# Optimization experiments

Measured on AMD Instinct MI355X. Metric: run time of the kernel, lower is better.

The kernel has to match this reference:

```python
import jax, jax.numpy as jnp
import numpy as np

S1, S2 = 1024, 1024
DA, DV, DOUT = 2, 64, 1
K1, K2 = 32, 32


def _gelu(x):
    # torch nn.GELU() default is the exact erf-based gelu
    return jax.nn.gelu(x, approximate=False)


def _flayer(Rr, Ri, w, x):
    f = jnp.fft.rfftn(x, axes=(0, 1))[:K1, :K2]            # [K1,K2,DV] complex
    Rf = jnp.einsum('abc,abcd->abd', f, Rr + 1j * Ri)       # [K1,K2,DV] complex
    kernelpart = jnp.fft.irfftn(Rf, s=(S1, S2), axes=(0, 1))  # [S1,S2,DV] real
    return _gelu(kernelpart + x @ w)


def setup_inputs() -> dict:
    key = jax.random.key(0)
    ks = jax.random.split(key, 20)
    d = {}
    d['input'] = jax.random.normal(ks[0], (S1, S2, DA), dtype=jnp.float32)
    d['Wsh'] = jax.random.normal(ks[1], (DA, DV), dtype=jnp.float32) * (1.0 / np.sqrt(DA))
    d['bsh'] = jax.random.normal(ks[2], (DV,), dtype=jnp.float32) * 0.02
    for i, base in zip(range(1, 5), range(3, 15, 3)):
        d[f'Rr{i}'] = jax.random.normal(ks[base], (K1, K2, DV, DV), dtype=jnp.float32) * (1.0 / DV)
        d[f'Ri{i}'] = jax.random.normal(ks[base + 1], (K1, K2, DV, DV), dtype=jnp.float32) * (1.0 / DV)
        d[f'w{i}'] = jax.random.normal(ks[base + 2], (DV, DV), dtype=jnp.float32) * (1.0 / np.sqrt(DV))
    d['Wp'] = jax.random.normal(ks[15], (DV, DOUT), dtype=jnp.float32) * (1.0 / np.sqrt(DV))
    d['bp'] = jax.random.normal(ks[16], (DOUT,), dtype=jnp.float32) * 0.02
    return d


def reference(input, Wsh, bsh, Rr1, Ri1, w1, Rr2, Ri2, w2,
              Rr3, Ri3, w3, Rr4, Ri4, w4, Wp, bp):
    vt = _gelu(input @ Wsh + bsh)          # Shallow: Linear + GELU
    vt = _flayer(Rr1, Ri1, w1, vt)
    vt = _flayer(Rr2, Ri2, w2, vt)
    vt = _flayer(Rr3, Ri3, w3, vt)
    vt = _flayer(Rr4, Ri4, w4, vt)
    u = (vt @ Wp + bp)[:, :, 0]            # Project, take channel 0 -> [S1,S2]
    return u
```

## Files before the change

kernel.cpp:

```cpp
#include <hip/hip_runtime.h>
#include <math.h>

#define MASKN 1023

typedef unsigned short ushort_t;
typedef __attribute__((ext_vector_type(8))) short short8;
typedef __attribute__((ext_vector_type(4))) float floatx4;
typedef __attribute__((ext_vector_type(4))) unsigned short us4v;

__device__ __forceinline__ float gelu_f(float x) {
    float x2 = x * x;
    float inner = fmaf(0.044715f * x, x2, x);
    float t = exp2f(inner * -2.302089214f);
    return x * __builtin_amdgcn_rcpf(1.0f + t);
}

__device__ __forceinline__ float bf2f(ushort_t h) {
    return __uint_as_float(((unsigned int)h) << 16);
}
__device__ __forceinline__ ushort_t f2bf(float f) {
    unsigned int u = __float_as_uint(f);
    u += 0x7FFFu + ((u >> 16) & 1u);
    return (ushort_t)(u >> 16);
}
struct us4 { ushort_t x, y, z, w; };

__device__ __forceinline__ unsigned int pk2bf(float lo, float hi) {
    unsigned int r;
    asm("v_cvt_pk_bf16_f32 %0, %1, %2" : "=v"(r) : "v"(lo), "v"(hi));
    return r;
}

__device__ __forceinline__ void st4(ushort_t* p, float4 v) {
    uint2 w;
    w.x = pk2bf(v.x, v.y);
    w.y = pk2bf(v.z, v.w);
    *(uint2*)p = w;
}

__device__ __forceinline__ void async16(ushort_t* l, const ushort_t* g) {
    __builtin_amdgcn_global_load_lds(
        (const __attribute__((address_space(1))) void*)g,
        (__attribute__((address_space(3))) void*)l, 16, 0, 0);
}

__global__ void k_fill_tw(float* __restrict__ ct, float* __restrict__ st) {
    int j = blockIdx.x * 256 + threadIdx.x;
    float ang = (float)j * (6.283185307179586f / 1024.0f);
    float s, c;
    sincosf(ang, &s, &c);
    ct[j] = c; st[j] = s;
}

__global__ void k_fill_T1(ushort_t* __restrict__ T1h, ushort_t* __restrict__ T1l) {
    int idx = blockIdx.x * 256 + threadIdx.x;
    int k2p = idx >> 10, y = idx & 1023;
    int k2 = k2p >> 1;
    float ang = (float)((k2 * y) & MASKN) * (6.283185307179586f / 1024.0f);
    float s, c;
    sincosf(ang, &s, &c);
    float v = (k2p & 1) ? -s : c;
    ushort_t h = f2bf(v);
    T1h[idx] = h;
    T1l[idx] = f2bf(v - bf2f(h));
}

__global__ void k_fill_T2(ushort_t* __restrict__ T2h, ushort_t* __restrict__ T2l) {
    int idx = blockIdx.x * 256 + threadIdx.x;
    int n2 = idx >> 6, kk = idx & 63;
    int k2 = kk >> 1;
    float ang = (float)((k2 * n2) & MASKN) * (6.283185307179586f / 1024.0f);
    float s, c;
    sincosf(ang, &s, &c);
    float v = (kk & 1) ? -s : c;
    ushort_t h = f2bf(v);
    T2h[idx] = h;
    T2l[idx] = f2bf(v - bf2f(h));
}

__global__ void k_fill_wT(const float* __restrict__ w1, const float* __restrict__ w2,
        const float* __restrict__ w3, const float* __restrict__ w4,
        ushort_t* __restrict__ wTh, ushort_t* __restrict__ wTl) {
    int l = blockIdx.y;
    int i = blockIdx.x * 256 + threadIdx.x;
    int d = i >> 6, c = i & 63;
    const float* w = (l == 0) ? w1 : (l == 1) ? w2 : (l == 2) ? w3 : w4;
    float v = w[c * 64 + d];
    ushort_t h = f2bf(v);
    wTh[l * 4096 + i] = h;
    wTl[l * 4096 + i] = f2bf(v - bf2f(h));
}

__global__ __launch_bounds__(256) void k_shallow(const float* __restrict__ in,
        const float* __restrict__ Wsh, const float* __restrict__ bsh,
        ushort_t* __restrict__ vt) {
    int tid = blockIdx.x * 256 + threadIdx.x;
    int p = tid >> 4, c0 = (tid & 15) << 2;
    float a0 = in[p * 2], a1 = in[p * 2 + 1];
    float4 w0 = *(const float4*)&Wsh[c0];
    float4 w1 = *(const float4*)&Wsh[64 + c0];
    float4 b  = *(const float4*)&bsh[c0];
    float4 r;
    r.x = gelu_f(fmaf(a0, w0.x, fmaf(a1, w1.x, b.x)));
    r.y = gelu_f(fmaf(a0, w0.y, fmaf(a1, w1.y, b.y)));
    r.z = gelu_f(fmaf(a0, w0.z, fmaf(a1, w1.z, b.z)));
    r.w = gelu_f(fmaf(a0, w0.w, fmaf(a1, w1.w, b.w)));
    st4(&vt[(size_t)p * 64 + c0], r);
}

#define VS1 72
__global__ __launch_bounds__(256, 3) void k_f1(const ushort_t* __restrict__ vt,
        const ushort_t* __restrict__ T1h, const ushort_t* __restrict__ T1l,
        float* __restrict__ gT) {
    __shared__ __align__(16) ushort_t t1s[2][8192];
    __shared__ __align__(16) ushort_t vs[2][64 * VS1];
    int t = threadIdx.x;
    int x = blockIdx.x;
    int wv = t >> 6, lane = t & 63;
    int lm = lane & 15, quad = lane >> 4;
    int lrow = t & 63, cq = (t >> 6) * 16;
    const ushort_t* vrow = vt + (size_t)x * 65536;

    floatx4 acc[4];
    #pragma unroll
    for (int nt = 0; nt < 4; ++nt) acc[nt] = (floatx4)(0.f);

    uint4 pf[2][2];
    #pragma unroll
    for (int i = 0; i < 4; ++i) {
        int j = (wv * 4 + i) * 64 + lane;
        int jj = j & 511;
        int r = jj >> 3, du = jj & 7, su = du ^ (r & 7);
        const ushort_t* src = ((j < 512) ? T1h : T1l) + (size_t)r * 1024 + su * 8;
        async16(&t1s[0][(wv * 4 + i) * 512], src);
    }
    __builtin_amdgcn_sched_barrier(0);
    {
        const ushort_t* s0 = vrow + (size_t)lrow * 64 + cq;
        pf[0][0] = *(const uint4*)(s0);
        pf[0][1] = *(const uint4*)(s0 + 8);
        const ushort_t* s1 = vrow + (size_t)(64 + lrow) * 64 + cq;
        pf[1][0] = *(const uint4*)(s1);
        pf[1][1] = *(const uint4*)(s1 + 8);
    }
    __builtin_amdgcn_sched_barrier(0);

    for (int hc = 0; hc < 16; ++hc) {
        int b = hc & 1;
        #pragma unroll
        for (int i = 0; i < 2; ++i) {
            union { uint4 u; ushort_t e[8]; } uv;
            uv.u = pf[b][i];
            #pragma unroll
            for (int j = 0; j < 8; ++j)
                vs[b][(cq + i * 8 + j) * VS1 + lrow] = uv.e[j];
        }
        __builtin_amdgcn_sched_barrier(0);
        if (hc < 15) asm volatile("s_waitcnt vmcnt(2)" ::: "memory");
        else         asm volatile("s_waitcnt vmcnt(0)" ::: "memory");
        __builtin_amdgcn_sched_barrier(0);
        __builtin_amdgcn_s_barrier();
        if (hc < 15) {
            #pragma unroll
            for (int i = 0; i < 4; ++i) {
                int j = (wv * 4 + i) * 64 + lane;
                int jj = j & 511;
                int r = jj >> 3, du = jj & 7, su = du ^ (r & 7);
                const ushort_t* src = ((j < 512) ? T1h : T1l)
                                      + (size_t)r * 1024 + (hc + 1) * 64 + su * 8;
                async16(&t1s[b ^ 1][(wv * 4 + i) * 512], src);
            }
        }
        if (hc < 14) {
            const ushort_t* srcv = vrow + (size_t)((hc + 2) * 64 + lrow) * 64 + cq;
            pf[b][0] = *(const uint4*)(srcv);
            pf[b][1] = *(const uint4*)(srcv + 8);
        }
        __builtin_amdgcn_sched_barrier(0);

        #pragma unroll
        for (int ys = 0; ys < 2; ++ys) {
            short8 af = *(const short8*)&vs[b][(wv * 16 + lm) * VS1 + ys * 32 + quad * 8];
            #pragma unroll
            for (int nt = 0; nt < 4; ++nt) {
                int sl = (((ys * 4 + quad) ^ (lm & 7)) * 8);
                short8 bh = *(const short8*)&t1s[b][(nt * 16 + lm) * 64 + sl];
                short8 bl = *(const short8*)&t1s[b][4096 + (nt * 16 + lm) * 64 + sl];
                acc[nt] = __builtin_amdgcn_mfma_f32_16x16x32_bf16(af, bh, acc[nt], 0, 0, 0);
                acc[nt] = __builtin_amdgcn_mfma_f32_16x16x32_bf16(af, bl, acc[nt], 0, 0, 0);
            }
        }
    }
    float* grow = gT + (size_t)x * 4096;
    #pragma unroll
    for (int nt = 0; nt < 4; ++nt)
        #pragma unroll
        for (int r = 0; r < 4; ++r)
            grow[(wv * 16 + quad * 4 + r) * 64 + nt * 16 + lm] = acc[nt][r];
}

__global__ __launch_bounds__(256) void k_f2(const float* __restrict__ gT,
        const float* __restrict__ ct, const float* __restrict__ st,
        float* __restrict__ fpr, float* __restrict__ fpi) {
    int t = threadIdx.x;
    int cx = blockIdx.x;
    int cg = blockIdx.y;
    int k10 = blockIdx.z * 8;
    int l = t & 63;
    int q = t >> 6;
    int c = cg * 4 + q;
    int e = l & 1;
    int k2 = l >> 1;
    float acc[8];
    #pragma unroll
    for (int i = 0; i < 8; ++i) acc[i] = 0.f;
    for (int xi = 0; xi < 128; ++xi) {
        int x = cx * 128 + xi;
        float v = gT[(size_t)x * 4096 + c * 64 + l];
        float p = __shfl_xor(v, 1);
        float gr = e ? p : v;
        float gi = e ? v : p;
        float u  = e ? gi : gr;
        float w2 = e ? -gr : gi;
        float cb = ct[x], sb = st[x];
        int ph = (x * k10) & MASKN;
        float cr = ct[ph], sr = st[ph];
        #pragma unroll
        for (int j = 0; j < 8; ++j) {
            acc[j] = fmaf(u, cr, fmaf(w2, sr, acc[j]));
            float nc = fmaf(cr, cb, -sr * sb);
            float ns = fmaf(sr, cb, cr * sb);
            cr = nc; sr = ns;
        }
    }
    float* dst = e ? fpi : fpr;
    #pragma unroll
    for (int j = 0; j < 8; ++j)
        dst[(size_t)cx * 65536 + ((k10 + j) * 32 + k2) * 64 + c] = acc[j];
}

__global__ __launch_bounds__(64) void k_mix(const float* __restrict__ fpr, const float* __restrict__ fpi,
        const float* __restrict__ Rr, const float* __restrict__ Ri,
        float* __restrict__ Rfr, float* __restrict__ Rfi) {
    __shared__ float fr[64], fi[64];
    int m = blockIdx.x;
    int d = threadIdx.x;
    float sr = 0.f, si = 0.f;
    #pragma unroll
    for (int ch = 0; ch < 8; ++ch) {
        sr += fpr[(size_t)ch * 65536 + m * 64 + d];
        si += fpi[(size_t)ch * 65536 + m * 64 + d];
    }
    fr[d] = sr; fi[d] = si;
    __syncthreads();
    const float* Rrb = Rr + (size_t)m * 4096;
    const float* Rib = Ri + (size_t)m * 4096;
    float ar = 0.f, ai = 0.f;
    for (int c = 0; c < 64; ++c) {
        float rr = Rrb[c * 64 + d], ri = Rib[c * 64 + d];
        ar = fmaf(fr[c], rr, fmaf(-fi[c], ri, ar));
        ai = fmaf(fr[c], ri, fmaf(fi[c], rr, ai));
    }
    Rfr[m * 64 + d] = ar;
    Rfi[m * 64 + d] = ai;
}

__global__ __launch_bounds__(256) void k_i1(const float* __restrict__ Rfr, const float* __restrict__ Rfi,
        const float* __restrict__ ctg, const float* __restrict__ stg,
        ushort_t* __restrict__ Bh, ushort_t* __restrict__ Bl) {
    __shared__ float ct[1024], st[1024];
    int t = threadIdx.x;
    #pragma unroll
    for (int i = 0; i < 4; ++i) { int j = t + 256 * i; ct[j] = ctg[j]; st[j] = stg[j]; }
    __syncthreads();
    int n1 = blockIdx.x;
    int d = t & 63;
    int k20 = (t >> 6) * 8;
    float br[8], bi[8];
    #pragma unroll
    for (int j = 0; j < 8; ++j) { br[j] = 0.f; bi[j] = 0.f; }
    int idx = 0;
    for (int k1 = 0; k1 < 32; ++k1) {
        float cc = ct[idx], ss = st[idx];
        idx = (idx + n1) & MASKN;
        #pragma unroll
        for (int j = 0; j < 8; ++j) {
            float rr = Rfr[(k1 * 32 + k20 + j) * 64 + d];
            float ri = Rfi[(k1 * 32 + k20 + j) * 64 + d];
            br[j] = fmaf(rr, cc, fmaf(-ri, ss, br[j]));
            bi[j] = fmaf(rr, ss, fmaf(ri, cc, bi[j]));
        }
    }
    union { uint4 u[2]; ushort_t e[16]; } hh, ll;
    #pragma unroll
    for (int j = 0; j < 8; ++j) {
        int k2 = k20 + j;
        float sc = (k2 == 0 ? 1.0f : 2.0f) * 9.5367431640625e-7f;
        float vr = br[j] * sc, vi = bi[j] * sc;
        ushort_t hr = f2bf(vr), hi2 = f2bf(vi);
        hh.e[2 * j] = hr;          hh.e[2 * j + 1] = hi2;
        ll.e[2 * j] = f2bf(vr - bf2f(hr));
        ll.e[2 * j + 1] = f2bf(vi - bf2f(hi2));
    }
    size_t base = ((size_t)n1 * 64 + d) * 64 + 2 * k20;
    *(uint4*)(Bh + base) = hh.u[0];
    *(uint4*)(Bh + base + 8) = hh.u[1];
    *(uint4*)(Bl + base) = ll.u[0];
    *(uint4*)(Bl + base + 8) = ll.u[1];
}

template<bool FINAL>
__global__ __launch_bounds__(256, 4) void k_i2(ushort_t* __restrict__ vt,
        const ushort_t* __restrict__ Bh, const ushort_t* __restrict__ Bl,
        const ushort_t* __restrict__ T2h, const ushort_t* __restrict__ T2l,
        const ushort_t* __restrict__ wTh, const ushort_t* __restrict__ wTl,
        const float* __restrict__ Wp, const float* __restrict__ bp,
        float* __restrict__ out) {
    __shared__ __align__(16) ushort_t ab[16384];
    int t = threadIdx.x;
    int wv = t >> 6, lane = t & 63;
    int lm = lane & 15, quad = lane >> 4;
    int n1 = blockIdx.x;
    const ushort_t* Bhr = Bh + (size_t)n1 * 4096;
    const ushort_t* Blr = Bl + (size_t)n1 * 4096;

    {
        const ushort_t* s = (wv == 0) ? Bhr : (wv == 1) ? Blr : (wv == 2) ? wTh : wTl;
        #pragma unroll
        for (int i = 0; i < 8; ++i) {
            int j = i * 64 + lane;
            int r = j >> 3, u = (j & 7) ^ (r & 7);
            async16(&ab[wv * 4096 + i * 512], s + r * 64 + u * 8);
        }
    }

    int n2b = wv * 16 + lm;
    const ushort_t* t2hp = T2h + n2b * 64 + quad * 8;
    const ushort_t* t2lp = T2l + n2b * 64 + quad * 8;
    const ushort_t* vrd  = vt + ((size_t)n1 * 1024 + n2b) * 64 + quad * 8;
    ushort_t*       vst  = vt + ((size_t)n1 * 1024 + n2b) * 64;

    short8 th[2][2], tl[2][2], vv[2][2];
    #pragma unroll
    for (int ks = 0; ks < 2; ++ks) {
        th[0][ks] = *(const short8*)(t2hp + ks * 32);
        tl[0][ks] = *(const short8*)(t2lp + ks * 32);
        vv[0][ks] = *(const short8*)(vrd + ks * 32);
    }
    float4 wpv[4];
    float bp0 = 0.f;
    if (FINAL) {
        bp0 = bp[0];
        #pragma unroll
        for (int mt = 0; mt < 4; ++mt) wpv[mt] = *(const float4*)&Wp[mt * 16 + quad * 4];
    }
    __syncthreads();

    int r7 = lm & 7;
    #pragma unroll
    for (int c = 0; c < 16; ++c) {
        if (c < 15) {
            #pragma unroll
            for (int ks = 0; ks < 2; ++ks) {
                th[(c + 1) & 1][ks] = *(const short8*)(t2hp + (c + 1) * 4096 + ks * 32);
                tl[(c + 1) & 1][ks] = *(const short8*)(t2lp + (c + 1) * 4096 + ks * 32);
                vv[(c + 1) & 1][ks] = *(const short8*)(vrd + (size_t)(c + 1) * 4096 + ks * 32);
            }
        }
        __builtin_amdgcn_sched_barrier(0);

        floatx4 acc[4];
        #pragma unroll
        for (int mt = 0; mt < 4; ++mt) acc[mt] = (floatx4)(0.f);

        __builtin_amdgcn_s_setprio(1);
        #pragma unroll
        for (int ks = 0; ks < 2; ++ks) {
            int sl = ((ks * 4 + quad) ^ r7) * 8;
            #pragma unroll
            for (int mt = 0; mt < 4; ++mt) {
                int ro = (mt * 16 + lm) * 64 + sl;
                short8 ah = *(const short8*)&ab[ro];
                short8 al = *(const short8*)&ab[4096 + ro];
                short8 wh = *(const short8*)&ab[8192 + ro];
                short8 wl = *(const short8*)&ab[12288 + ro];
                acc[mt] = __builtin_amdgcn_mfma_f32_16x16x32_bf16(ah, th[c & 1][ks], acc[mt], 0, 0, 0);
                acc[mt] = __builtin_amdgcn_mfma_f32_16x16x32_bf16(al, th[c & 1][ks], acc[mt], 0, 0, 0);
                acc[mt] = __builtin_amdgcn_mfma_f32_16x16x32_bf16(ah, tl[c & 1][ks], acc[mt], 0, 0, 0);
                acc[mt] = __builtin_amdgcn_mfma_f32_16x16x32_bf16(wh, vv[c & 1][ks], acc[mt], 0, 0, 0);
                acc[mt] = __builtin_amdgcn_mfma_f32_16x16x32_bf16(wl, vv[c & 1][ks], acc[mt], 0, 0, 0);
            }
        }
        __builtin_amdgcn_s_setprio(0);

        if (!FINAL) {
            #pragma unroll
            for (int mt = 0; mt < 4; ++mt) {
                uint2 w;
                w.x = pk2bf(gelu_f(acc[mt][0]), gelu_f(acc[mt][1]));
                w.y = pk2bf(gelu_f(acc[mt][2]), gelu_f(acc[mt][3]));
                *(uint2*)(vst + (size_t)c * 4096 + mt * 16 + quad * 4) = w;
            }
        } else {
            float s = 0.f;
            #pragma unroll
            for (int mt = 0; mt < 4; ++mt) {
                s = fmaf(gelu_f(acc[mt][0]), wpv[mt].x, s);
                s = fmaf(gelu_f(acc[mt][1]), wpv[mt].y, s);
                s = fmaf(gelu_f(acc[mt][2]), wpv[mt].z, s);
                s = fmaf(gelu_f(acc[mt][3]), wpv[mt].w, s);
            }
            s += __shfl_xor(s, 16);
            s += __shfl_xor(s, 32);
            if (quad == 0)
                out[(size_t)n1 * 1024 + c * 64 + n2b] = s + bp0;
        }
    }
}

extern "C" void kernel_launch(void* const* d_in, const int* in_sizes, int n_in,
                              void* d_out, int out_size, void* d_ws, size_t ws_size,
                              hipStream_t stream) {
    const float* in  = (const float*)d_in[0];
    const float* Wsh = (const float*)d_in[1];
    const float* bsh = (const float*)d_in[2];
    const float* Wp  = (const float*)d_in[15];
    const float* bp  = (const float*)d_in[16];

    char* wsb = (char*)d_ws;
    ushort_t* vt   = (ushort_t*)wsb;
    float* ctab = (float*)(wsb + 134217728);
    float* stab = ctab + 1024;
    float* gT   = stab + 1024;
    float* Rfr  = gT + 4194304;
    float* Rfi  = Rfr + 65536;
    ushort_t* T1h = (ushort_t*)(Rfi + 65536);
    ushort_t* T1l = T1h + 65536;
    ushort_t* T2h = T1l + 65536;
    ushort_t* T2l = T2h + 65536;
    ushort_t* wTh = T2l + 65536;
    ushort_t* wTl = wTh + 16384;
    ushort_t* Bh  = (ushort_t*)gT;
    ushort_t* Bl  = Bh + 4194304;
    float* fpr = (float*)d_out;
    float* fpi = fpr + 524288;

    k_fill_tw<<<4, 256, 0, stream>>>(ctab, stab);
    k_fill_T1<<<256, 256, 0, stream>>>(T1h, T1l);
    k_fill_T2<<<256, 256, 0, stream>>>(T2h, T2l);
    k_fill_wT<<<dim3(16, 4), 256, 0, stream>>>((const float*)d_in[5], (const float*)d_in[8],
                                               (const float*)d_in[11], (const float*)d_in[14], wTh, wTl);
    k_shallow<<<65536, 256, 0, stream>>>(in, Wsh, bsh, vt);
    for (int L = 0; L < 4; ++L) {
        const float* Rr = (const float*)d_in[3 + L * 3];
        const float* Ri = (const float*)d_in[4 + L * 3];
        k_f1<<<1024, 256, 0, stream>>>(vt, T1h, T1l, gT);
        k_f2<<<dim3(8, 16, 4), 256, 0, stream>>>(gT, ctab, stab, fpr, fpi);
        k_mix<<<1024, 64, 0, stream>>>(fpr, fpi, Rr, Ri, Rfr, Rfi);
        k_i1<<<1024, 256, 0, stream>>>(Rfr, Rfi, ctab, stab, Bh, Bl);
        if (L < 3) {
            k_i2<false><<<1024, 256, 0, stream>>>(vt, Bh, Bl, T2h, T2l,
                    wTh + L * 4096, wTl + L * 4096, nullptr, nullptr, nullptr);
        } else {
            k_i2<true><<<1024, 256, 0, stream>>>(vt, Bh, Bl, T2h, T2l,
                    wTh + L * 4096, wTl + L * 4096, Wp, bp, (float*)d_out);
        }
    }
}
```

Measured before the change: 773.4 us.

## Exploit even/odd k2 symmetry to halve inverse-DFT twiddle work in k_i2

The final inverse DFT over n2 is split into even and odd k2 terms, using the fact that shifting n2 by 512 leaves the even-k2 twiddles unchanged and flips the sign of the odd-k2 twiddles. Each block now computes outputs for n2 and n2+512 together as E+O and E-O, so spectral MFMA work and T2 table loads are halved. The B layout and T2 table are reordered into even/odd halves to match, and the T2 table shrinks to 512 rows. The pointwise w-matmul is still done for both halves, so register pressure grows because of four accumulator sets.

```diff
diff --git a/kernel.cpp b/kernel.cpp
--- a/kernel.cpp
+++ b/kernel.cpp
@@ -67,12 +67,13 @@
 
 __global__ void k_fill_T2(ushort_t* __restrict__ T2h, ushort_t* __restrict__ T2l) {
     int idx = blockIdx.x * 256 + threadIdx.x;
-    int n2 = idx >> 6, kk = idx & 63;
-    int k2 = kk >> 1;
+    int n2 = idx >> 6, col = idx & 63;
+    int w = col & 31;
+    int k2 = ((w >> 1) << 1) + (col >> 5);
     float ang = (float)((k2 * n2) & MASKN) * (6.283185307179586f / 1024.0f);
     float s, c;
     sincosf(ang, &s, &c);
-    float v = (kk & 1) ? -s : c;
+    float v = (w & 1) ? -s : c;
     ushort_t h = f2bf(v);
     T2h[idx] = h;
     T2l[idx] = f2bf(v - bf2f(h));
@@ -291,22 +292,23 @@
             bi[j] = fmaf(rr, ss, fmaf(ri, cc, bi[j]));
         }
     }
-    union { uint4 u[2]; ushort_t e[16]; } hh, ll;
+    union { uint4 u; ushort_t e[8]; } he, ho, le, lo_;
     #pragma unroll
     for (int j = 0; j < 8; ++j) {
         int k2 = k20 + j;
         float sc = (k2 == 0 ? 1.0f : 2.0f) * 9.5367431640625e-7f;
         float vr = br[j] * sc, vi = bi[j] * sc;
         ushort_t hr = f2bf(vr), hi2 = f2bf(vi);
-        hh.e[2 * j] = hr;          hh.e[2 * j + 1] = hi2;
-        ll.e[2 * j] = f2bf(vr - bf2f(hr));
-        ll.e[2 * j + 1] = f2bf(vi - bf2f(hi2));
-    }
-    size_t base = ((size_t)n1 * 64 + d) * 64 + 2 * k20;
-    *(uint4*)(Bh + base) = hh.u[0];
-    *(uint4*)(Bh + base + 8) = hh.u[1];
-    *(uint4*)(Bl + base) = ll.u[0];
-    *(uint4*)(Bl + base + 8) = ll.u[1];
+        ushort_t lr = f2bf(vr - bf2f(hr)), li = f2bf(vi - bf2f(hi2));
+        int p = (j >> 1) << 1;
+        if (j & 1) { ho.e[p] = hr; ho.e[p + 1] = hi2; lo_.e[p] = lr; lo_.e[p + 1] = li; }
+        else       { he.e[p] = hr; he.e[p + 1] = hi2; le.e[p]  = lr; le.e[p + 1]  = li; }
+    }
+    size_t base = ((size_t)n1 * 64 + d) * 64;
+    *(uint4*)(Bh + base + k20)      = he.u;
+    *(uint4*)(Bh + base + 32 + k20) = ho.u;
+    *(uint4*)(Bl + base + k20)      = le.u;
+    *(uint4*)(Bl + base + 32 + k20) = lo_.u;
 }
 
 template<bool FINAL>
@@ -335,17 +337,22 @@
     }
 
     int n2b = wv * 16 + lm;
-    const ushort_t* t2hp = T2h + n2b * 64 + quad * 8;
-    const ushort_t* t2lp = T2l + n2b * 64 + quad * 8;
-    const ushort_t* vrd  = vt + ((size_t)n1 * 1024 + n2b) * 64 + quad * 8;
-    ushort_t*       vst  = vt + ((size_t)n1 * 1024 + n2b) * 64;
-
-    short8 th[2][2], tl[2][2], vv[2][2];
+    const ushort_t* t2hb = T2h + (size_t)n2b * 64 + quad * 8;
+    const ushort_t* t2lb = T2l + (size_t)n2b * 64 + quad * 8;
+    const ushort_t* vrdL = vt + ((size_t)n1 * 1024 + n2b) * 64 + quad * 8;
+    const ushort_t* vrdH = vrdL + 32768;
+    ushort_t*       vstL = vt + ((size_t)n1 * 1024 + n2b) * 64;
+    ushort_t*       vstH = vstL + 32768;
+
+    short8 the[2], tho[2], tle[2], tlo[2], vL[2][2], vH[2][2];
+    the[0] = *(const short8*)(t2hb);
+    tho[0] = *(const short8*)(t2hb + 32);
+    tle[0] = *(const short8*)(t2lb);
+    tlo[0] = *(const short8*)(t2lb + 32);
     #pragma unroll
     for (int ks = 0; ks < 2; ++ks) {
-        th[0][ks] = *(const short8*)(t2hp + ks * 32);
-        tl[0][ks] = *(const short8*)(t2lp + ks * 32);
-        vv[0][ks] = *(const short8*)(vrd + ks * 32);
+        vL[0][ks] = *(const short8*)(vrdL + ks * 32);
+        vH[0][ks] = *(const short8*)(vrdH + ks * 32);
     }
     float4 wpv[4];
     float bp0 = 0.f;
@@ -358,37 +365,61 @@
 
     int r7 = lm & 7;
     #pragma unroll
-    for (int c = 0; c < 16; ++c) {
-        if (c < 15) {
+    for (int c = 0; c < 8; ++c) {
+        int b = c & 1;
+        if (c < 7) {
+            int nb = b ^ 1;
             #pragma unroll
             for (int ks = 0; ks < 2; ++ks) {
-                th[(c + 1) & 1][ks] = *(const short8*)(t2hp + (c + 1) * 4096 + ks * 32);
-                tl[(c + 1) & 1][ks] = *(const short8*)(t2lp + (c + 1) * 4096 + ks * 32);
-                vv[(c + 1) & 1][ks] = *(const short8*)(vrd + (size_t)(c + 1) * 4096 + ks * 32);
-            }
+                vL[nb][ks] = *(const short8*)(vrdL + (size_t)(c + 1) * 4096 + ks * 32);
+                vH[nb][ks] = *(const short8*)(vrdH + (size_t)(c + 1) * 4096 + ks * 32);
+            }
+            the[nb] = *(const short8*)(t2hb + (c + 1) * 4096);
+            tho[nb] = *(const short8*)(t2hb + (c + 1) * 4096 + 32);
+            tle[nb] = *(const short8*)(t2lb + (c + 1) * 4096);
+            tlo[nb] = *(const short8*)(t2lb + (c + 1) * 4096 + 32);
         }
         __builtin_amdgcn_sched_barrier(0);
 
-        floatx4 acc[4];
-        #pragma unroll
-        for (int mt = 0; mt < 4; ++mt) acc[mt] = (floatx4)(0.f);
+        floatx4 aE[4], aO[4], aL[4], aH[4];
+        #pragma unroll
+        for (int mt = 0; mt < 4; ++mt) {
+            aE[mt] = (floatx4)(0.f); aO[mt] = (floatx4)(0.f);
+            aL[mt] = (floatx4)(0.f); aH[mt] = (floatx4)(0.f);
+        }
 
         __builtin_amdgcn_s_setprio(1);
+        {
+            int slE = (quad ^ r7) * 8;
+            int slO = ((4 + quad) ^ r7) * 8;
+            #pragma unroll
+            for (int mt = 0; mt < 4; ++mt) {
+                int roE = (mt * 16 + lm) * 64 + slE;
+                int roO = (mt * 16 + lm) * 64 + slO;
+                short8 aeh = *(const short8*)&ab[roE];
+                short8 ael = *(const short8*)&ab[4096 + roE];
+                short8 aoh = *(const short8*)&ab[roO];
+                short8 aol = *(const short8*)&ab[4096 + roO];
+                aE[mt] = __builtin_amdgcn_mfma_f32_16x16x32_bf16(aeh, the[b], aE[mt], 0, 0, 0);
+                aE[mt] = __builtin_amdgcn_mfma_f32_16x16x32_bf16(ael, the[b], aE[mt], 0, 0, 0);
+                aE[mt] = __builtin_amdgcn_mfma_f32_16x16x32_bf16(aeh, tle[b], aE[mt], 0, 0, 0);
+                aO[mt] = __builtin_amdgcn_mfma_f32_16x16x32_bf16(aoh, tho[b], aO[mt], 0, 0, 0);
+                aO[mt] = __builtin_amdgcn_mfma_f32_16x16x32_bf16(aol, tho[b], aO[mt], 0, 0, 0);
+                aO[mt] = __builtin_amdgcn_mfma_f32_16x16x32_bf16(aoh, tlo[b], aO[mt], 0, 0, 0);
+            }
+        }
         #pragma unroll
         for (int ks = 0; ks < 2; ++ks) {
             int sl = ((ks * 4 + quad) ^ r7) * 8;
             #pragma unroll
             for (int mt = 0; mt < 4; ++mt) {
                 int ro = (mt * 16 + lm) * 64 + sl;
-                short8 ah = *(const short8*)&ab[ro];
-                short8 al = *(const short8*)&ab[4096 + ro];
                 short8 wh = *(const short8*)&ab[8192 + ro];
                 short8 wl = *(const short8*)&ab[12288 + ro];
-                acc[mt] = __builtin_amdgcn_mfma_f32_16x16x32_bf16(ah, th[c & 1][ks], acc[mt], 0, 0, 0);
-                acc[mt] = __builtin_amdgcn_mfma_f32_16x16x32_bf16(al, th[c & 1][ks], acc[mt], 0, 0, 0);
-                acc[mt] = __builtin_amdgcn_mfma_f32_16x16x32_bf16(ah, tl[c & 1][ks], acc[mt], 0, 0, 0);
-                acc[mt] = __builtin_amdgcn_mfma_f32_16x16x32_bf16(wh, vv[c & 1][ks], acc[mt], 0, 0, 0);
-                acc[mt] = __builtin_amdgcn_mfma_f32_16x16x32_bf16(wl, vv[c & 1][ks], acc[mt], 0, 0, 0);
+                aL[mt] = __builtin_amdgcn_mfma_f32_16x16x32_bf16(wh, vL[b][ks], aL[mt], 0, 0, 0);
+                aL[mt] = __builtin_amdgcn_mfma_f32_16x16x32_bf16(wl, vL[b][ks], aL[mt], 0, 0, 0);
+                aH[mt] = __builtin_amdgcn_mfma_f32_16x16x32_bf16(wh, vH[b][ks], aH[mt], 0, 0, 0);
+                aH[mt] = __builtin_amdgcn_mfma_f32_16x16x32_bf16(wl, vH[b][ks], aH[mt], 0, 0, 0);
             }
         }
         __builtin_amdgcn_s_setprio(0);
@@ -396,24 +427,37 @@
         if (!FINAL) {
             #pragma unroll
             for (int mt = 0; mt < 4; ++mt) {
-                uint2 w;
-                w.x = pk2bf(gelu_f(acc[mt][0]), gelu_f(acc[mt][1]));
-                w.y = pk2bf(gelu_f(acc[mt][2]), gelu_f(acc[mt][3]));
-                *(uint2*)(vst + (size_t)c * 4096 + mt * 16 + quad * 4) = w;
+                floatx4 lo4 = aE[mt] + aO[mt] + aL[mt];
+                floatx4 hi4 = aE[mt] - aO[mt] + aH[mt];
+                uint2 wlo, whi;
+                wlo.x = pk2bf(gelu_f(lo4[0]), gelu_f(lo4[1]));
+                wlo.y = pk2bf(gelu_f(lo4[2]), gelu_f(lo4[3]));
+                whi.x = pk2bf(gelu_f(hi4[0]), gelu_f(hi4[1]));
+                whi.y = pk2bf(gelu_f(hi4[2]), gelu_f(hi4[3]));
+                *(uint2*)(vstL + (size_t)c * 4096 + mt * 16 + quad * 4) = wlo;
+                *(uint2*)(vstH + (size_t)c * 4096 + mt * 16 + quad * 4) = whi;
             }
         } else {
-            float s = 0.f;
+            float sL = 0.f, sH = 0.f;
             #pragma unroll
             for (int mt = 0; mt < 4; ++mt) {
-                s = fmaf(gelu_f(acc[mt][0]), wpv[mt].x, s);
-                s = fmaf(gelu_f(acc[mt][1]), wpv[mt].y, s);
-                s = fmaf(gelu_f(acc[mt][2]), wpv[mt].z, s);
-                s = fmaf(gelu_f(acc[mt][3]), wpv[mt].w, s);
-            }
-            s += __shfl_xor(s, 16);
-            s += __shfl_xor(s, 32);
-            if (quad == 0)
-                out[(size_t)n1 * 1024 + c * 64 + n2b] = s + bp0;
+                floatx4 lo4 = aE[mt] + aO[mt] + aL[mt];
+                floatx4 hi4 = aE[mt] - aO[mt] + aH[mt];
+                sL = fmaf(gelu_f(lo4[0]), wpv[mt].x, sL);
+                sL = fmaf(gelu_f(lo4[1]), wpv[mt].y, sL);
+                sL = fmaf(gelu_f(lo4[2]), wpv[mt].z, sL);
+                sL = fmaf(gelu_f(lo4[3]), wpv[mt].w, sL);
+                sH = fmaf(gelu_f(hi4[0]), wpv[mt].x, sH);
+                sH = fmaf(gelu_f(hi4[1]), wpv[mt].y, sH);
+                sH = fmaf(gelu_f(hi4[2]), wpv[mt].z, sH);
+                sH = fmaf(gelu_f(hi4[3]), wpv[mt].w, sH);
+            }
+            sL += __shfl_xor(sL, 16); sL += __shfl_xor(sL, 32);
+            sH += __shfl_xor(sH, 16); sH += __shfl_xor(sH, 32);
+            if (quad == 0) {
+                out[(size_t)n1 * 1024 + c * 64 + n2b] = sL + bp0;
+                out[(size_t)n1 * 1024 + 512 + c * 64 + n2b] = sH + bp0;
+            }
         }
     }
 }
@@ -447,7 +491,7 @@
 
     k_fill_tw<<<4, 256, 0, stream>>>(ctab, stab);
     k_fill_T1<<<256, 256, 0, stream>>>(T1h, T1l);
-    k_fill_T2<<<256, 256, 0, stream>>>(T2h, T2l);
+    k_fill_T2<<<128, 256, 0, stream>>>(T2h, T2l);
     k_fill_wT<<<dim3(16, 4), 256, 0, stream>>>((const float*)d_in[5], (const float*)d_in[8],
                                                (const float*)d_in[11], (const float*)d_in[14], wTh, wTl);
     k_shallow<<<65536, 256, 0, stream>>>(in, Wsh, bsh, vt);
```

Result: slower. 808.5 us (+4.5%).

## Process two x-rows per k_f1 block to reuse loaded twiddle tiles

Applied to the files above, without the earlier changes.

Each k_f1 block now handles two consecutive rows of vt instead of one. The T1 twiddle tiles loaded into shared memory are shared by both rows, so twiddle traffic per row is halved. The grid shrinks to 512 blocks, and the per-block register and LDS footprint grows, so the occupancy hint drops from 3 to 2 blocks. This risks less latency hiding and fewer blocks to spread across CUs, in exchange for less global and LDS load traffic per MFMA.

```diff
diff --git a/kernel.cpp b/kernel.cpp
--- a/kernel.cpp
+++ b/kernel.cpp
@@ -109,23 +109,26 @@
 }
 
 #define VS1 72
-__global__ __launch_bounds__(256, 3) void k_f1(const ushort_t* __restrict__ vt,
+__global__ __launch_bounds__(256, 2) void k_f1(const ushort_t* __restrict__ vt,
         const ushort_t* __restrict__ T1h, const ushort_t* __restrict__ T1l,
         float* __restrict__ gT) {
     __shared__ __align__(16) ushort_t t1s[2][8192];
-    __shared__ __align__(16) ushort_t vs[2][64 * VS1];
+    __shared__ __align__(16) ushort_t vs[2][2][64 * VS1];
     int t = threadIdx.x;
-    int x = blockIdx.x;
+    int x0 = blockIdx.x * 2;
     int wv = t >> 6, lane = t & 63;
     int lm = lane & 15, quad = lane >> 4;
     int lrow = t & 63, cq = (t >> 6) * 16;
-    const ushort_t* vrow = vt + (size_t)x * 65536;
-
-    floatx4 acc[4];
-    #pragma unroll
-    for (int nt = 0; nt < 4; ++nt) acc[nt] = (floatx4)(0.f);
-
-    uint4 pf[2][2];
+    const ushort_t* vrow0 = vt + (size_t)x0 * 65536;
+    const ushort_t* vrow1 = vrow0 + 65536;
+
+    floatx4 acc[2][4];
+    #pragma unroll
+    for (int xi = 0; xi < 2; ++xi)
+        #pragma unroll
+        for (int nt = 0; nt < 4; ++nt) acc[xi][nt] = (floatx4)(0.f);
+
+    uint4 pf[2][2][2];
     #pragma unroll
     for (int i = 0; i < 4; ++i) {
         int j = (wv * 4 + i) * 64 + lane;
@@ -136,27 +139,35 @@
     }
     __builtin_amdgcn_sched_barrier(0);
     {
-        const ushort_t* s0 = vrow + (size_t)lrow * 64 + cq;
-        pf[0][0] = *(const uint4*)(s0);
-        pf[0][1] = *(const uint4*)(s0 + 8);
-        const ushort_t* s1 = vrow + (size_t)(64 + lrow) * 64 + cq;
-        pf[1][0] = *(const uint4*)(s1);
-        pf[1][1] = *(const uint4*)(s1 + 8);
+        const ushort_t* s00 = vrow0 + (size_t)lrow * 64 + cq;
+        pf[0][0][0] = *(const uint4*)(s00);
+        pf[0][0][1] = *(const uint4*)(s00 + 8);
+        const ushort_t* s01 = vrow1 + (size_t)lrow * 64 + cq;
+        pf[0][1][0] = *(const uint4*)(s01);
+        pf[0][1][1] = *(const uint4*)(s01 + 8);
+        const ushort_t* s10 = vrow0 + (size_t)(64 + lrow) * 64 + cq;
+        pf[1][0][0] = *(const uint4*)(s10);
+        pf[1][0][1] = *(const uint4*)(s10 + 8);
+        const ushort_t* s11 = vrow1 + (size_t)(64 + lrow) * 64 + cq;
+        pf[1][1][0] = *(const uint4*)(s11);
+        pf[1][1][1] = *(const uint4*)(s11 + 8);
     }
     __builtin_amdgcn_sched_barrier(0);
 
     for (int hc = 0; hc < 16; ++hc) {
         int b = hc & 1;
         #pragma unroll
-        for (int i = 0; i < 2; ++i) {
-            union { uint4 u; ushort_t e[8]; } uv;
-            uv.u = pf[b][i];
-            #pragma unroll
-            for (int j = 0; j < 8; ++j)
-                vs[b][(cq + i * 8 + j) * VS1 + lrow] = uv.e[j];
-        }
+        for (int xi = 0; xi < 2; ++xi)
+            #pragma unroll
+            for (int i = 0; i < 2; ++i) {
+                union { uint4 u; ushort_t e[8]; } uv;
+                uv.u = pf[b][xi][i];
+                #pragma unroll
+                for (int j = 0; j < 8; ++j)
+                    vs[b][xi][(cq + i * 8 + j) * VS1 + lrow] = uv.e[j];
+            }
         __builtin_amdgcn_sched_barrier(0);
-        if (hc < 15) asm volatile("s_waitcnt vmcnt(2)" ::: "memory");
+        if (hc < 15) asm volatile("s_waitcnt vmcnt(4)" ::: "memory");
         else         asm volatile("s_waitcnt vmcnt(0)" ::: "memory");
         __builtin_amdgcn_sched_barrier(0);
         __builtin_amdgcn_s_barrier();
@@ -172,31 +183,40 @@
             }
         }
         if (hc < 14) {
-            const ushort_t* srcv = vrow + (size_t)((hc + 2) * 64 + lrow) * 64 + cq;
-            pf[b][0] = *(const uint4*)(srcv);
-            pf[b][1] = *(const uint4*)(srcv + 8);
+            const ushort_t* s0 = vrow0 + (size_t)((hc + 2) * 64 + lrow) * 64 + cq;
+            pf[b][0][0] = *(const uint4*)(s0);
+            pf[b][0][1] = *(const uint4*)(s0 + 8);
+            const ushort_t* s1 = vrow1 + (size_t)((hc + 2) * 64 + lrow) * 64 + cq;
+            pf[b][1][0] = *(const uint4*)(s1);
+            pf[b][1][1] = *(const uint4*)(s1 + 8);
         }
         __builtin_amdgcn_sched_barrier(0);
 
         #pragma unroll
         for (int ys = 0; ys < 2; ++ys) {
-            short8 af = *(const short8*)&vs[b][(wv * 16 + lm) * VS1 + ys * 32 + quad * 8];
+            short8 af0 = *(const short8*)&vs[b][0][(wv * 16 + lm) * VS1 + ys * 32 + quad * 8];
+            short8 af1 = *(const short8*)&vs[b][1][(wv * 16 + lm) * VS1 + ys * 32 + quad * 8];
             #pragma unroll
             for (int nt = 0; nt < 4; ++nt) {
                 int sl = (((ys * 4 + quad) ^ (lm & 7)) * 8);
                 short8 bh = *(const short8*)&t1s[b][(nt * 16 + lm) * 64 + sl];
                 short8 bl = *(const short8*)&t1s[b][4096 + (nt * 16 + lm) * 64 + sl];
-                acc[nt] = __builtin_amdgcn_mfma_f32_16x16x32_bf16(af, bh, acc[nt], 0, 0, 0);
-                acc[nt] = __builtin_amdgcn_mfma_f32_16x16x32_bf16(af, bl, acc[nt], 0, 0, 0);
-            }
-        }
-    }
-    float* grow = gT + (size_t)x * 4096;
-    #pragma unroll
-    for (int nt = 0; nt < 4; ++nt)
-        #pragma unroll
-        for (int r = 0; r < 4; ++r)
-            grow[(wv * 16 + quad * 4 + r) * 64 + nt * 16 + lm] = acc[nt][r];
+                acc[0][nt] = __builtin_amdgcn_mfma_f32_16x16x32_bf16(af0, bh, acc[0][nt], 0, 0, 0);
+                acc[0][nt] = __builtin_amdgcn_mfma_f32_16x16x32_bf16(af0, bl, acc[0][nt], 0, 0, 0);
+                acc[1][nt] = __builtin_amdgcn_mfma_f32_16x16x32_bf16(af1, bh, acc[1][nt], 0, 0, 0);
+                acc[1][nt] = __builtin_amdgcn_mfma_f32_16x16x32_bf16(af1, bl, acc[1][nt], 0, 0, 0);
+            }
+        }
+    }
+    #pragma unroll
+    for (int xi = 0; xi < 2; ++xi) {
+        float* grow = gT + (size_t)(x0 + xi) * 4096;
+        #pragma unroll
+        for (int nt = 0; nt < 4; ++nt)
+            #pragma unroll
+            for (int r = 0; r < 4; ++r)
+                grow[(wv * 16 + quad * 4 + r) * 64 + nt * 16 + lm] = acc[xi][nt][r];
+    }
 }
 
 __global__ __launch_bounds__(256) void k_f2(const float* __restrict__ gT,
@@ -454,7 +474,7 @@
     for (int L = 0; L < 4; ++L) {
         const float* Rr = (const float*)d_in[3 + L * 3];
         const float* Ri = (const float*)d_in[4 + L * 3];
-        k_f1<<<1024, 256, 0, stream>>>(vt, T1h, T1l, gT);
+        k_f1<<<512, 256, 0, stream>>>(vt, T1h, T1l, gT);
         k_f2<<<dim3(8, 16, 4), 256, 0, stream>>>(gT, ctab, stab, fpr, fpi);
         k_mix<<<1024, 64, 0, stream>>>(fpr, fpi, Rr, Ri, Rfr, Rfi);
         k_i1<<<1024, 256, 0, stream>>>(Rfr, Rfi, ctab, stab, Bh, Bl);
```

Result: faster. 733.5 us (-5.2%).
